# Kernel optimization log

Hardware: AMD Instinct MI355X
Metric: run time of the kernel (lower is better)

Reference implementation:

```python
import jax, jax.numpy as jnp
import numpy as np

N, E, F, H, HEADS, L, G, NC = 50000, 800000, 128, 64, 4, 3, 64, 2
EPS = 1e-5


def _init(key, shape, fan_in):
    return jax.random.normal(key, shape, jnp.float32) / np.sqrt(fan_in)


def setup_inputs() -> dict:
    key = jax.random.key(0)
    ks = jax.random.split(key, 24)
    x = jax.random.normal(ks[0], (N, F), jnp.float32)
    edge_index = jax.random.randint(ks[1], (2, E), 0, N, jnp.int32)
    batch = jnp.sort(jax.random.randint(ks[2], (N,), 0, G, jnp.int32))
    return {
        "x": x, "edge_index": edge_index, "batch": batch,
        "Wi": _init(ks[3], (F, H), F), "bi": jnp.zeros((H,), jnp.float32),
        "gcn_W": _init(ks[4], (L, H, H), H), "gcn_b": jnp.zeros((L, H), jnp.float32),
        "gcn_gamma": jnp.ones((L, H), jnp.float32), "gcn_beta": jnp.zeros((L, H), jnp.float32),
        "Wg": _init(ks[5], (H, HEADS * H), H), "bg": jnp.zeros((H,), jnp.float32),
        "att_src": _init(ks[6], (HEADS, H), H), "att_dst": _init(ks[7], (HEADS, H), H),
        "gat_gamma": jnp.ones((H,), jnp.float32), "gat_beta": jnp.zeros((H,), jnp.float32),
        "c1_W": _init(ks[8], (2 * H, H), 2 * H), "c1_b": jnp.zeros((H,), jnp.float32),
        "c2_W": _init(ks[9], (H, H // 2), H), "c2_b": jnp.zeros((H // 2,), jnp.float32),
        "c3_W": _init(ks[10], (H // 2, NC), H // 2), "c3_b": jnp.zeros((NC,), jnp.float32),
    }


def _batch_norm(x, gamma, beta):
    # training-mode BN over the node dimension
    mu = x.mean(0)
    var = x.var(0)
    return (x - mu) * jax.lax.rsqrt(var + EPS) * gamma + beta


def _gcn_conv(x, W, b, src, dst):
    # PyG GCNConv: add self loops + symmetric normalization D^-1/2 (A+I) D^-1/2
    h = x @ W  # [N, H]
    ones = jnp.ones((src.shape[0],), h.dtype)
    deg = jax.ops.segment_sum(ones, dst, num_segments=N) + 1.0  # +1 for self loop
    dinv = jax.lax.rsqrt(deg)
    norm = dinv[src] * dinv[dst]  # [E]
    out = jax.ops.segment_sum(h[src] * norm[:, None], dst, num_segments=N)
    out = out + h * (dinv * dinv)[:, None]  # self-loop term: deg^-1
    return out + b


def _gat_conv(x, W, att_s, att_d, b, src, dst):
    # PyG GATConv, concat=False (mean over heads), leaky_relu slope 0.2, self loops
    h = (x @ W).reshape(N, HEADS, H)  # [N, Hd, C]
    a_s = (h * att_s).sum(-1)  # [N, Hd]
    a_d = (h * att_d).sum(-1)
    sl = jnp.arange(N, dtype=src.dtype)
    si = jnp.concatenate([src, sl])
    di = jnp.concatenate([dst, sl])
    logits = jax.nn.leaky_relu(a_s[si] + a_d[di], 0.2)  # [E+N, Hd]
    # segment softmax over destination node per head
    m = jax.ops.segment_max(logits, di, num_segments=N)  # every node has a self loop
    e = jnp.exp(logits - m[di])
    s = jax.ops.segment_sum(e, di, num_segments=N)
    alpha = e / (s[di] + 1e-16)  # [E+N, Hd]
    out = jax.ops.segment_sum(h[si] * alpha[:, :, None], di, num_segments=N)  # [N, Hd, C]
    return out.mean(axis=1) + b


def reference(x, edge_index, batch, Wi, bi, gcn_W, gcn_b, gcn_gamma, gcn_beta,
              Wg, bg, att_src, att_dst, gat_gamma, gat_beta,
              c1_W, c1_b, c2_W, c2_b, c3_W, c3_b):
    src, dst = edge_index[0], edge_index[1]
    h = jax.nn.relu(x @ Wi + bi)
    for l in range(L):
        identity = h
        h = _gcn_conv(h, gcn_W[l], gcn_b[l], src, dst)
        h = _batch_norm(h, gcn_gamma[l], gcn_beta[l])
        h = jax.nn.relu(h)  # dropout: eval mode (identity)
        h = h + identity
    identity = h
    h = _gat_conv(h, Wg, att_src, att_dst, bg, src, dst)
    h = _batch_norm(h, gat_gamma, gat_beta)
    h = jax.nn.elu(h)
    h = h + identity
    # dual pooling over graphs
    cnt = jax.ops.segment_sum(jnp.ones((N,), h.dtype), batch, num_segments=G,
                              indices_are_sorted=True)
    x_mean = jax.ops.segment_sum(h, batch, num_segments=G, indices_are_sorted=True)
    x_mean = x_mean / jnp.maximum(cnt, 1.0)[:, None]
    x_max = jax.ops.segment_max(h, batch, num_segments=G, indices_are_sorted=True)
    x_max = jnp.where(jnp.isfinite(x_max), x_max, 0.0)
    z = jnp.concatenate([x_mean, x_max], axis=1)  # [G, 2H]
    z = jax.nn.relu(z @ c1_W + c1_b)
    z = jax.nn.relu(z @ c2_W + c2_b)
    return z @ c3_W + c3_b  # [G, NC]
```

## Files before the change

kernel.cpp:

```cpp
#include <hip/hip_runtime.h>
#include <math.h>

#define N_ 50000
#define E_ 800000
#define F_ 128
#define H_ 64
#define G_ 64
#define NC_ 2
#define CAP_ 96
#define EPS_ 1e-5f
#define GRID_P 1250
#define BNSLOTS 64
#define WIS_STRIDE 136
#define W0_STRIDE 72
#define WGS 72

typedef _Float16 f16;
typedef f16 f16x2 __attribute__((ext_vector_type(2)));
typedef f16 f16x4 __attribute__((ext_vector_type(4)));
typedef f16 f16x8 __attribute__((ext_vector_type(8)));
typedef unsigned short u16;
typedef u16 u16x8 __attribute__((ext_vector_type(8)));

__device__ __forceinline__ unsigned fkey(float f) {
    unsigned u = __float_as_uint(f);
    return (u & 0x80000000u) ? ~u : (u | 0x80000000u);
}
__device__ __forceinline__ float funkey(unsigned k) {
    unsigned u = (k & 0x80000000u) ? (k & 0x7fffffffu) : ~k;
    return __uint_as_float(u);
}
__device__ __forceinline__ float leaky(float x) { return x > 0.f ? x : 0.2f * x; }

__device__ __forceinline__ void dot8(const f16x8 w, const f16x8 v,
                                     float& a0, float& a1, float& a2, float& a3) {
    a0 = __builtin_amdgcn_fdot2(__builtin_shufflevector(w, w, 0, 1),
                                __builtin_shufflevector(v, v, 0, 1), a0, false);
    a1 = __builtin_amdgcn_fdot2(__builtin_shufflevector(w, w, 2, 3),
                                __builtin_shufflevector(v, v, 2, 3), a1, false);
    a2 = __builtin_amdgcn_fdot2(__builtin_shufflevector(w, w, 4, 5),
                                __builtin_shufflevector(v, v, 4, 5), a2, false);
    a3 = __builtin_amdgcn_fdot2(__builtin_shufflevector(w, w, 6, 7),
                                __builtin_shufflevector(v, v, 6, 7), a3, false);
}

__device__ __forceinline__ void stat_reduce(const float* __restrict__ part,
                                            float* statb) {
    int t = threadIdx.x;
    if (t < 128) {
        float s = 0.f;
#pragma unroll
        for (int b = 0; b < BNSLOTS; b++) s += part[b * 128 + t];
        statb[t] = s;
    }
    __syncthreads();
    if (t < H_) {
        float mu = statb[t] / (float)N_;
        float var = statb[H_ + t] / (float)N_ - mu * mu;
        statb[t] = mu;
        statb[H_ + t] = rsqrtf(var + EPS_);
    }
    __syncthreads();
}

__global__ void k_fill(const int* __restrict__ ei, int* __restrict__ rowcnt,
                       u16* __restrict__ slotS) {
    int e = blockIdx.x * 256 + threadIdx.x;
    if (e >= E_) return;
    int d = ei[E_ + e];
    int pos = atomicAdd(&rowcnt[d], 1);
    if (pos < CAP_) slotS[d * CAP_ + pos] = (u16)ei[e];
}

__global__ __launch_bounds__(256) void k_in_mm(const float* __restrict__ x,
                                               const float* __restrict__ Wi,
                                               const float* __restrict__ bi,
                                               const float* __restrict__ W0,
                                               const int* __restrict__ rowcnt,
                                               float* __restrict__ hA,
                                               f16* __restrict__ hWs) {
    __shared__ __attribute__((aligned(16))) f16 Wis[H_ * WIS_STRIDE];
    __shared__ __attribute__((aligned(16))) f16 W0s[H_ * W0_STRIDE];
    __shared__ __attribute__((aligned(16))) f16 xb[4 * F_];
    __shared__ __attribute__((aligned(16))) f16 rb[4 * H_];
    int tid = threadIdx.x;
    for (int i = tid; i < F_ * H_; i += 256) {
        int k = i >> 6, j = i & 63;
        Wis[j * WIS_STRIDE + k] = (f16)Wi[i];
    }
    for (int i = tid; i < H_ * H_; i += 256) {
        int k = i >> 6, j = i & 63;
        W0s[j * W0_STRIDE + k] = (f16)W0[i];
    }
    __syncthreads();
    int r = tid >> 6, j = tid & 63;
    float bj = bi[j];
    const f16* wc1 = Wis + j * WIS_STRIDE;
    const f16* wc2 = W0s + j * W0_STRIDE;
    f16* xr = xb + r * F_;
    f16* rr = rb + r * H_;
    int grp = blockIdx.x;
    float2 xv = *(const float2*)&x[(size_t)(grp * 4 + r) * F_ + 2 * j];
    for (; grp < N_ / 4; grp += GRID_P) {
        f16x2 xs = {(f16)xv.x, (f16)xv.y};
        *(f16x2*)&xr[2 * j] = xs;
        int ng = grp + GRID_P;
        if (ng < N_ / 4)
            xv = *(const float2*)&x[(size_t)(ng * 4 + r) * F_ + 2 * j];
        int n = grp * 4 + r;
        float a0 = 0.f, a1 = 0.f, a2 = 0.f, a3 = 0.f;
#pragma unroll
        for (int k = 0; k < F_; k += 8)
            dot8(*(const f16x8*)&wc1[k], *(const f16x8*)&xr[k], a0, a1, a2, a3);
        float y = fmaxf((a0 + a1) + (a2 + a3) + bj, 0.f);
        hA[(size_t)n * H_ + j] = y;
        rr[j] = (f16)y;
        float b0 = 0.f, b1 = 0.f, b2 = 0.f, b3 = 0.f;
#pragma unroll
        for (int k = 0; k < H_; k += 8)
            dot8(*(const f16x8*)&wc2[k], *(const f16x8*)&rr[k], b0, b1, b2, b3);
        hWs[(size_t)n * H_ + j] =
            (f16)(((b0 + b1) + (b2 + b3)) * rsqrtf((float)rowcnt[n] + 1.f));
    }
}

__global__ __launch_bounds__(256) void k_gcn_gather(const int* __restrict__ rowcnt,
                                                    const u16* __restrict__ slotS,
                                                    const f16* __restrict__ hWs,
                                                    float* __restrict__ out,
                                                    float* __restrict__ bnpart) {
    __shared__ float st[4][128];
    int r = threadIdx.x >> 6;
    int d = blockIdx.x * 4 + r;
    int L = threadIdx.x & 63;
    int rg = L >> 4, q = L & 15;
    int rc = rowcnt[d];
    int cnt = min(rc, CAP_);
    float dd = rsqrtf((float)rc + 1.f);
    size_t base = (size_t)d * CAP_;
    float a0 = 0.f, a1 = 0.f, a2 = 0.f, a3 = 0.f;
    if (rg == 0) {
        f16x4 hv = *(const f16x4*)&hWs[(size_t)d * H_ + q * 4];
        a0 = (float)hv[0]; a1 = (float)hv[1]; a2 = (float)hv[2]; a3 = (float)hv[3];
    }
    for (int k = 0; k < cnt; k += 16) {
        u16x8 iA = *(const u16x8*)&slotS[base + k];
        u16x8 iB = *(const u16x8*)&slotS[base + k + 8];
        int e = k + rg;
        int s0 = (e < cnt) ? (int)iA[rg] : d;
        int s1 = (e + 4 < cnt) ? (int)iA[4 + rg] : d;
        int s2 = (e + 8 < cnt) ? (int)iB[rg] : d;
        int s3 = (e + 12 < cnt) ? (int)iB[4 + rg] : d;
        f16x4 v0 = *(const f16x4*)&hWs[(size_t)s0 * H_ + q * 4];
        f16x4 v1 = *(const f16x4*)&hWs[(size_t)s1 * H_ + q * 4];
        f16x4 v2 = *(const f16x4*)&hWs[(size_t)s2 * H_ + q * 4];
        f16x4 v3 = *(const f16x4*)&hWs[(size_t)s3 * H_ + q * 4];
        float m0 = (e < cnt) ? 1.f : 0.f;
        float m1 = (e + 4 < cnt) ? 1.f : 0.f;
        float m2 = (e + 8 < cnt) ? 1.f : 0.f;
        float m3 = (e + 12 < cnt) ? 1.f : 0.f;
        a0 += (m0 * (float)v0[0] + m1 * (float)v1[0]) +
              (m2 * (float)v2[0] + m3 * (float)v3[0]);
        a1 += (m0 * (float)v0[1] + m1 * (float)v1[1]) +
              (m2 * (float)v2[1] + m3 * (float)v3[1]);
        a2 += (m0 * (float)v0[2] + m1 * (float)v1[2]) +
              (m2 * (float)v2[2] + m3 * (float)v3[2]);
        a3 += (m0 * (float)v0[3] + m1 * (float)v1[3]) +
              (m2 * (float)v2[3] + m3 * (float)v3[3]);
    }
    a0 += __shfl_xor(a0, 16); a0 += __shfl_xor(a0, 32);
    a1 += __shfl_xor(a1, 16); a1 += __shfl_xor(a1, 32);
    a2 += __shfl_xor(a2, 16); a2 += __shfl_xor(a2, 32);
    a3 += __shfl_xor(a3, 16); a3 += __shfl_xor(a3, 32);
    if (rg == 0) {
        float y0 = a0 * dd, y1 = a1 * dd, y2 = a2 * dd, y3 = a3 * dd;
        *(float4*)&out[(size_t)d * H_ + q * 4] = make_float4(y0, y1, y2, y3);
        st[r][q * 4 + 0] = y0;  st[r][64 + q * 4 + 0] = y0 * y0;
        st[r][q * 4 + 1] = y1;  st[r][64 + q * 4 + 1] = y1 * y1;
        st[r][q * 4 + 2] = y2;  st[r][64 + q * 4 + 2] = y2 * y2;
        st[r][q * 4 + 3] = y3;  st[r][64 + q * 4 + 3] = y3 * y3;
    }
    __syncthreads();
    for (int t = threadIdx.x; t < 128; t += 256) {
        float vsum = (st[0][t] + st[1][t]) + (st[2][t] + st[3][t]);
        atomicAdd(&bnpart[(blockIdx.x & (BNSLOTS - 1)) * 128 + t], vsum);
    }
}

__global__ __launch_bounds__(256) void k_bn_mm(const float* __restrict__ v,
                                               const float* __restrict__ bnpart,
                                               const float* __restrict__ gamma,
                                               const float* __restrict__ beta,
                                               const float* __restrict__ res,
                                               const float* __restrict__ W,
                                               const int* __restrict__ rowcnt,
                                               float* __restrict__ out_res,
                                               f16* __restrict__ hWs) {
    __shared__ __attribute__((aligned(16))) f16 Ws[H_ * W0_STRIDE];
    __shared__ __attribute__((aligned(16))) f16 rb[4 * H_];
    __shared__ float statb[128];
    int tid = threadIdx.x;
    for (int i = tid; i < H_ * H_; i += 256) {
        int k = i >> 6, j = i & 63;
        Ws[j * W0_STRIDE + k] = (f16)W[i];
    }
    stat_reduce(bnpart, statb);
    int r = tid >> 6, j = tid & 63;
    float mu = statb[j], rs = statb[H_ + j], ga = gamma[j], be = beta[j];
    const f16* wc = Ws + j * W0_STRIDE;
    f16* rr = rb + r * H_;
    for (int grp = blockIdx.x; grp < N_ / 4; grp += GRID_P) {
        int n = grp * 4 + r;
        size_t idx = (size_t)n * H_ + j;
        float y = (v[idx] - mu) * rs * ga + be;
        y = fmaxf(y, 0.f) + res[idx];
        out_res[idx] = y;
        rr[j] = (f16)y;
        float b0 = 0.f, b1 = 0.f, b2 = 0.f, b3 = 0.f;
#pragma unroll
        for (int k = 0; k < H_; k += 8)
            dot8(*(const f16x8*)&wc[k], *(const f16x8*)&rr[k], b0, b1, b2, b3);
        hWs[idx] = (f16)(((b0 + b1) + (b2 + b3)) * rsqrtf((float)rowcnt[n] + 1.f));
    }
}

__global__ __launch_bounds__(256) void k_wg(const float* __restrict__ v,
                                            const float* __restrict__ bnpart,
                                            const float* __restrict__ gamma,
                                            const float* __restrict__ beta,
                                            const float* __restrict__ res,
                                            const float* __restrict__ Wg,
                                            const float* __restrict__ asw,
                                            const float* __restrict__ adw,
                                            float* __restrict__ hOut,
                                            f16* __restrict__ hg16,
                                            float* __restrict__ a_s,
                                            float* __restrict__ a_d) {
    __shared__ __attribute__((aligned(16))) f16 Wgs[256 * WGS];
    __shared__ __attribute__((aligned(16))) f16 xb[32 * H_];
    __shared__ float statb[128];
    int tid = threadIdx.x;
    for (int i = tid; i < H_ * 256; i += 256) {
        int k = i >> 8, j = i & 255;
        Wgs[j * WGS + k] = (f16)Wg[i];
    }
    stat_reduce(bnpart, statb);
    int n0 = blockIdx.x * 32;
    int nrows = min(32, N_ - n0);
    {
        int c = tid & 63;
        float mu = statb[c], rs = statb[H_ + c], ga = gamma[c], be = beta[c];
        for (int i = tid; i < nrows * H_; i += 256) {
            size_t idx = (size_t)n0 * H_ + i;
            float y = (v[idx] - mu) * rs * ga + be;
            y = fmaxf(y, 0.f) + res[idx];
            hOut[idx] = y;
            xb[i] = (f16)y;
        }
    }
    __syncthreads();
    int j = tid, wid = j >> 6, lane = j & 63;
    float aw = asw[j], dw = adw[j];
    const f16* wcol = &Wgs[j * WGS];
    for (int nn = 0; nn < nrows; nn++) {
        const f16* hr = xb + nn * H_;
        float a0 = 0.f, a1 = 0.f, a2 = 0.f, a3 = 0.f;
#pragma unroll
        for (int k = 0; k < H_; k += 8)
            dot8(*(const f16x8*)&wcol[k], *(const f16x8*)&hr[k], a0, a1, a2, a3);
        float acc = (a0 + a1) + (a2 + a3);
        int n = n0 + nn;
        hg16[(size_t)n * 256 + j] = (f16)acc;
        float ps = acc * aw, pd = acc * dw;
        for (int m = 1; m < 64; m <<= 1) {
            ps += __shfl_xor(ps, m);
            pd += __shfl_xor(pd, m);
        }
        if (lane == 0) { a_s[n * 4 + wid] = ps; a_d[n * 4 + wid] = pd; }
    }
}

__global__ __launch_bounds__(256) void k_gat(const int* __restrict__ rowcnt,
                                             const u16* __restrict__ slotS,
                                             const f16* __restrict__ hg16,
                                             const float* __restrict__ a_s,
                                             const float* __restrict__ a_d,
                                             float* __restrict__ out,
                                             float* __restrict__ bnpart) {
    __shared__ float st[4][128];
    int r = threadIdx.x >> 6;
    int d = blockIdx.x * 4 + r;
    int L = threadIdx.x & 63;
    int rg = L >> 5, p = L & 31;
    int h = p >> 3, o = p & 7;
    int cnt = min(rowcnt[d], CAP_);
    size_t base = (size_t)d * CAP_;
    float ads = a_d[d * 4 + h];
    float es = __expf(fminf(leaky(a_s[d * 4 + h] + ads), 19.f) - 8.f);
    float s = 0.f;
    float acc[8];
#pragma unroll
    for (int i = 0; i < 8; i++) acc[i] = 0.f;
    if (rg == 0) {
        s = es;
        f16x8 hv = *(const f16x8*)&hg16[(size_t)d * 256 + p * 8];
#pragma unroll
        for (int i = 0; i < 8; i++) acc[i] = es * (float)hv[i];
    }
    int k = 0;
    for (; k + 8 <= cnt; k += 8) {
        u16x8 iA = *(const u16x8*)&slotS[base + k];
        int s0 = (int)iA[rg];
        int s1 = (int)iA[2 + rg];
        int s2 = (int)iA[4 + rg];
        int s3 = (int)iA[6 + rg];
        float x0 = a_s[s0 * 4 + h];
        float x1 = a_s[s1 * 4 + h];
        float x2 = a_s[s2 * 4 + h];
        float x3 = a_s[s3 * 4 + h];
        f16x8 v0 = *(const f16x8*)&hg16[(size_t)s0 * 256 + p * 8];
        f16x8 v1 = *(const f16x8*)&hg16[(size_t)s1 * 256 + p * 8];
        f16x8 v2 = *(const f16x8*)&hg16[(size_t)s2 * 256 + p * 8];
        f16x8 v3 = *(const f16x8*)&hg16[(size_t)s3 * 256 + p * 8];
        float t0 = __expf(fminf(leaky(x0 + ads), 19.f) - 8.f);
        float t1 = __expf(fminf(leaky(x1 + ads), 19.f) - 8.f);
        float t2 = __expf(fminf(leaky(x2 + ads), 19.f) - 8.f);
        float t3 = __expf(fminf(leaky(x3 + ads), 19.f) - 8.f);
        s += (t0 + t1) + (t2 + t3);
#pragma unroll
        for (int i = 0; i < 8; i++)
            acc[i] += (t0 * (float)v0[i] + t1 * (float)v1[i]) +
                      (t2 * (float)v2[i] + t3 * (float)v3[i]);
    }
    for (; k < cnt; k += 2) {
        if (k + rg < cnt) {
            int sE = (int)slotS[base + k + rg];
            float t = __expf(fminf(leaky(a_s[sE * 4 + h] + ads), 19.f) - 8.f);
            f16x8 v = *(const f16x8*)&hg16[(size_t)sE * 256 + p * 8];
            s += t;
#pragma unroll
            for (int i = 0; i < 8; i++) acc[i] += t * (float)v[i];
        }
    }
    s += __shfl_xor(s, 32);
#pragma unroll
    for (int i = 0; i < 8; i++) acc[i] += __shfl_xor(acc[i], 32);
    float w = 0.25f / (s + 1e-16f);
#pragma unroll
    for (int i = 0; i < 8; i++) acc[i] *= w;
#pragma unroll
    for (int i = 0; i < 8; i++) {
        acc[i] += __shfl_xor(acc[i], 8);
        acc[i] += __shfl_xor(acc[i], 16);
    }
    if (L < 8) {
        float4 oA = make_float4(acc[0], acc[1], acc[2], acc[3]);
        float4 oB = make_float4(acc[4], acc[5], acc[6], acc[7]);
        *(float4*)&out[(size_t)d * H_ + o * 8] = oA;
        *(float4*)&out[(size_t)d * H_ + o * 8 + 4] = oB;
#pragma unroll
        for (int i = 0; i < 8; i++) {
            st[r][o * 8 + i] = acc[i];
            st[r][64 + o * 8 + i] = acc[i] * acc[i];
        }
    }
    __syncthreads();
    for (int t = threadIdx.x; t < 128; t += 256) {
        float vsum = (st[0][t] + st[1][t]) + (st[2][t] + st[3][t]);
        atomicAdd(&bnpart[(blockIdx.x & (BNSLOTS - 1)) * 128 + t], vsum);
    }
}

__global__ __launch_bounds__(256) void k_pool_bn(const float* __restrict__ accv,
                                                 const float* __restrict__ bnpart,
                                                 const float* __restrict__ gamma,
                                                 const float* __restrict__ beta,
                                                 const float* __restrict__ res,
                                                 const int* __restrict__ batch,
                                                 float* __restrict__ xmean,
                                                 unsigned int* __restrict__ xmaxb,
                                                 float* __restrict__ cnt) {
    __shared__ float statb[128];
    stat_reduce(bnpart, statb);
    const int CH = 196;
    int n0 = blockIdx.x * CH;
    int nEnd = min(n0 + CH, N_);
    int c = threadIdx.x & 63, r = threadIdx.x >> 6;
    float mu = statb[c], rs = statb[H_ + c], ga = gamma[c], be = beta[c];
    int curg = -1, cc = 0;
    float s = 0.f;
    unsigned mk = 0u;
    for (int n = n0 + r; n < nEnd; n += 4) {
        int g = batch[n];
        if (g != curg) {
            if (curg >= 0) {
                atomicAdd(&xmean[curg * H_ + c], s);
                atomicMax(&xmaxb[curg * H_ + c], mk);
                if (c == 0) atomicAdd(&cnt[curg], (float)cc);
            }
            curg = g; s = 0.f; mk = 0u; cc = 0;
        }
        size_t idx = (size_t)n * H_ + c;
        float y = (accv[idx] - mu) * rs * ga + be;
        y = (y > 0.f ? y : expf(y) - 1.f) + res[idx];
        s += y;
        unsigned kv = fkey(y);
        mk = mk > kv ? mk : kv;
        cc++;
    }
    if (curg >= 0) {
        atomicAdd(&xmean[curg * H_ + c], s);
        atomicMax(&xmaxb[curg * H_ + c], mk);
        if (c == 0) atomicAdd(&cnt[curg], (float)cc);
    }
}

__global__ __launch_bounds__(64) void k_head(const float* __restrict__ xmean,
                                             const unsigned int* __restrict__ xmaxb,
                                             const float* __restrict__ cnt,
                                             const float* __restrict__ c1W, const float* __restrict__ c1b,
                                             const float* __restrict__ c2W, const float* __restrict__ c2b,
                                             const float* __restrict__ c3W, const float* __restrict__ c3b,
                                             float* __restrict__ out) {
    __shared__ float z[2 * H_];
    __shared__ float o1[H_];
    __shared__ float o2[32];
    int g = blockIdx.x, j = threadIdx.x;
    float cn = fmaxf(cnt[g], 1.f);
    z[j] = xmean[g * H_ + j] / cn;
    unsigned key = xmaxb[g * H_ + j];
    z[H_ + j] = (key == 0u) ? 0.f : funkey(key);
    __syncthreads();
    float a0 = c1b[j], a1 = 0.f, a2 = 0.f, a3 = 0.f;
    for (int k = 0; k < 2 * H_; k += 4) {
        a0 += z[k] * c1W[k * 64 + j];
        a1 += z[k + 1] * c1W[(k + 1) * 64 + j];
        a2 += z[k + 2] * c1W[(k + 2) * 64 + j];
        a3 += z[k + 3] * c1W[(k + 3) * 64 + j];
    }
    o1[j] = fmaxf((a0 + a1) + (a2 + a3), 0.f);
    __syncthreads();
    if (j < 32) {
        float b0 = c2b[j], b1 = 0.f, b2 = 0.f, b3 = 0.f;
        for (int k = 0; k < H_; k += 4) {
            b0 += o1[k] * c2W[k * 32 + j];
            b1 += o1[k + 1] * c2W[(k + 1) * 32 + j];
            b2 += o1[k + 2] * c2W[(k + 2) * 32 + j];
            b3 += o1[k + 3] * c2W[(k + 3) * 32 + j];
        }
        o2[j] = fmaxf((b0 + b1) + (b2 + b3), 0.f);
    }
    __syncthreads();
    if (j < NC_) {
        float c0 = c3b[j];
        for (int k = 0; k < 32; k++) c0 += o2[k] * c3W[k * 2 + j];
        out[g * NC_ + j] = c0;
    }
}

extern "C" void kernel_launch(void* const* d_in, const int* in_sizes, int n_in,
                              void* d_out, int out_size, void* d_ws, size_t ws_size,
                              hipStream_t stream) {
    const float* x     = (const float*)d_in[0];
    const int*   ei    = (const int*)d_in[1];
    const int*   batch = (const int*)d_in[2];
    const float* Wi    = (const float*)d_in[3];
    const float* bi    = (const float*)d_in[4];
    const float* gcnW  = (const float*)d_in[5];
    const float* gcnG  = (const float*)d_in[7];
    const float* gcnB  = (const float*)d_in[8];
    const float* Wg    = (const float*)d_in[9];
    const float* attS  = (const float*)d_in[11];
    const float* attD  = (const float*)d_in[12];
    const float* gatG  = (const float*)d_in[13];
    const float* gatB  = (const float*)d_in[14];
    const float* c1W   = (const float*)d_in[15];
    const float* c1b   = (const float*)d_in[16];
    const float* c2W   = (const float*)d_in[17];
    const float* c2b   = (const float*)d_in[18];
    const float* c3W   = (const float*)d_in[19];
    const float* c3b   = (const float*)d_in[20];
    float* out = (float*)d_out;

    float* p = (float*)d_ws;
    float* hA    = p; p += (size_t)N_ * H_;
    float* hB    = p; p += (size_t)N_ * H_;
    float* acc   = p; p += (size_t)N_ * H_;
    f16*   hg16  = (f16*)p; p += (size_t)N_ * 128;
    float* a_s   = p; p += (size_t)N_ * 4;
    float* a_d   = p; p += (size_t)N_ * 4;
    int* rowcnt = (int*)p; p += N_;
    float* bnpart4 = p; p += 4 * BNSLOTS * 128;
    float* xmean  = p; p += G_ * H_;
    unsigned int* xmaxb = (unsigned int*)p; p += G_ * H_;
    float* cnt = p; p += G_;
    const size_t ZWORDS = (size_t)N_ + 4 * BNSLOTS * 128 + G_ * H_ * 2 + G_;
    u16* slotS = (u16*)p; p += (size_t)N_ * CAP_ / 2 + 8;
    f16* hWs = (f16*)hg16;

    float* bnp0 = bnpart4;
    float* bnp1 = bnpart4 + 1 * BNSLOTS * 128;
    float* bnp2 = bnpart4 + 2 * BNSLOTS * 128;
    float* bnp3 = bnpart4 + 3 * BNSLOTS * 128;

    const int NB_E = (E_ + 255) / 256;
    const int NB_W = N_ / 4;

    hipMemsetAsync(rowcnt, 0, ZWORDS * sizeof(float), stream);
    k_fill<<<NB_E, 256, 0, stream>>>(ei, rowcnt, slotS);

    k_in_mm<<<GRID_P, 256, 0, stream>>>(x, Wi, bi, gcnW, rowcnt, hA, hWs);

    k_gcn_gather<<<NB_W, 256, 0, stream>>>(rowcnt, slotS, hWs, acc, bnp0);
    k_bn_mm<<<GRID_P, 256, 0, stream>>>(acc, bnp0, gcnG, gcnB, hA,
                                        gcnW + (size_t)1 * H_ * H_, rowcnt, hB, hWs);
    k_gcn_gather<<<NB_W, 256, 0, stream>>>(rowcnt, slotS, hWs, acc, bnp1);
    k_bn_mm<<<GRID_P, 256, 0, stream>>>(acc, bnp1, gcnG + H_, gcnB + H_, hB,
                                        gcnW + (size_t)2 * H_ * H_, rowcnt, hA, hWs);
    k_gcn_gather<<<NB_W, 256, 0, stream>>>(rowcnt, slotS, hWs, acc, bnp2);

    k_wg<<<(N_ + 31) / 32, 256, 0, stream>>>(acc, bnp2, gcnG + 2 * H_, gcnB + 2 * H_,
                                             hA, Wg, attS, attD, hB, hg16, a_s, a_d);
    k_gat<<<NB_W, 256, 0, stream>>>(rowcnt, slotS, hg16, a_s, a_d, acc, bnp3);

    k_pool_bn<<<256, 256, 0, stream>>>(acc, bnp3, gatG, gatB, hB, batch,
                                       xmean, xmaxb, cnt);

    k_head<<<G_, 64, 0, stream>>>(xmean, xmaxb, cnt, c1W, c1b, c2W, c2b, c3W, c3b, out);
}
```

Baseline: 438.7 us.

## Keep Wg columns in registers and fold attention vectors into Wg

Each thread now loads its Wg column into registers as fp16 instead of staging a transposed Wg copy in LDS, which removes a large shared-memory buffer and raises potential occupancy. The per-node attention logits are no longer taken as a wave-wide shuffle reduction of the transformed features. Instead the attention vectors are precomputed as Wg·att (a 64x8 matrix) and dotted directly with the input rows. This removes the per-row 6-step shuffle reductions, but every block redundantly recomputes the small folded matrix. The logits also change numerically: they now come from fp16 inputs with fp32 weights rather than from fp32 accumulated outputs.

```diff
diff --git a/kernel.cpp b/kernel.cpp
--- a/kernel.cpp
+++ b/kernel.cpp
@@ -13,7 +13,6 @@
 #define BNSLOTS 64
 #define WIS_STRIDE 136
 #define W0_STRIDE 72
-#define WGS 72
 
 typedef _Float16 f16;
 typedef f16 f16x2 __attribute__((ext_vector_type(2)));
@@ -236,13 +235,34 @@
                                             f16* __restrict__ hg16,
                                             float* __restrict__ a_s,
                                             float* __restrict__ a_d) {
-    __shared__ __attribute__((aligned(16))) f16 Wgs[256 * WGS];
     __shared__ __attribute__((aligned(16))) f16 xb[32 * H_];
     __shared__ float statb[128];
+    __shared__ float wsdL[8 * H_];
     int tid = threadIdx.x;
-    for (int i = tid; i < H_ * 256; i += 256) {
-        int k = i >> 8, j = i & 255;
-        Wgs[j * WGS + k] = (f16)Wg[i];
+    int j = tid;
+    f16x8 wreg[8];
+#pragma unroll
+    for (int kk = 0; kk < 8; kk++) {
+        f16x8 w;
+#pragma unroll
+        for (int i = 0; i < 8; i++)
+            w[i] = (f16)Wg[(size_t)(kk * 8 + i) * 256 + j];
+        wreg[kk] = w;
+    }
+    {
+        int k = tid >> 2, hd = tid & 3;
+        const float* wr = Wg + (size_t)k * 256 + hd * 64;
+        const float* asp = asw + hd * 64;
+        const float* adp = adw + hd * 64;
+        float ss = 0.f, dd = 0.f;
+#pragma unroll 8
+        for (int c = 0; c < 64; c++) {
+            float wv = wr[c];
+            ss += wv * asp[c];
+            dd += wv * adp[c];
+        }
+        wsdL[hd * 64 + k] = ss;
+        wsdL[(4 + hd) * 64 + k] = dd;
     }
     stat_reduce(bnpart, statb);
     int n0 = blockIdx.x * 32;
@@ -259,24 +279,32 @@
         }
     }
     __syncthreads();
-    int j = tid, wid = j >> 6, lane = j & 63;
-    float aw = asw[j], dw = adw[j];
-    const f16* wcol = &Wgs[j * WGS];
     for (int nn = 0; nn < nrows; nn++) {
         const f16* hr = xb + nn * H_;
         float a0 = 0.f, a1 = 0.f, a2 = 0.f, a3 = 0.f;
 #pragma unroll
-        for (int k = 0; k < H_; k += 8)
-            dot8(*(const f16x8*)&wcol[k], *(const f16x8*)&hr[k], a0, a1, a2, a3);
-        float acc = (a0 + a1) + (a2 + a3);
-        int n = n0 + nn;
-        hg16[(size_t)n * 256 + j] = (f16)acc;
-        float ps = acc * aw, pd = acc * dw;
-        for (int m = 1; m < 64; m <<= 1) {
-            ps += __shfl_xor(ps, m);
-            pd += __shfl_xor(pd, m);
-        }
-        if (lane == 0) { a_s[n * 4 + wid] = ps; a_d[n * 4 + wid] = pd; }
+        for (int kk = 0; kk < 8; kk++)
+            dot8(wreg[kk], *(const f16x8*)&hr[kk * 8], a0, a1, a2, a3);
+        hg16[(size_t)(n0 + nn) * 256 + j] = (f16)((a0 + a1) + (a2 + a3));
+    }
+    {
+        int row = tid >> 3, o = tid & 7;
+        if (row < nrows) {
+            const f16* hr = xb + row * H_;
+            const float* wcol = wsdL + o * 64;
+            float s0 = 0.f, s1 = 0.f, s2 = 0.f, s3 = 0.f;
+#pragma unroll
+            for (int c = 0; c < 64; c += 4) {
+                s0 += (float)hr[c] * wcol[c];
+                s1 += (float)hr[c + 1] * wcol[c + 1];
+                s2 += (float)hr[c + 2] * wcol[c + 2];
+                s3 += (float)hr[c + 3] * wcol[c + 3];
+            }
+            float val = (s0 + s1) + (s2 + s3);
+            int n = n0 + row;
+            if (o < 4) a_s[n * 4 + o] = val;
+            else       a_d[n * 4 + (o - 4)] = val;
+        }
     }
 }
 
```

Result: slower. 460.5 us (+5.0%).
